# Optimization experiments

Hardware: AMD Instinct MI355X
Metric: run time of the kernel (lower is better)

Reference implementation:

```python
import jax, jax.numpy as jnp
import numpy as np


def setup_inputs() -> dict:
    key = jax.random.key(0)
    kx, kw = jax.random.split(key)
    B, C, L = 8, 512, 4096
    WC, KS = 64, 7
    x = jax.random.normal(kx, (B, C, L), dtype=jnp.float32)
    w = jax.random.normal(kw, (B, WC, KS, L), dtype=jnp.float32)
    return {"x": x, "w": w}


def reference(x, w):
    # x: [B, C, L]; w: [B, WC, KS, L]; dynamic grouped depthwise 1D conv.
    B, C, L = x.shape
    _, WC, KS, _ = w.shape
    groups = C // WC
    pad = (KS - 1) // 2
    xp = jnp.pad(x, ((0, 0), (0, 0), (pad, pad)))  # [B, C, L+2*pad]
    # repeat_interleave along channel dim: output channel c uses w channel c // groups
    wf = jnp.repeat(w, groups, axis=1) if groups > 1 else w  # [B, C, KS, L]
    # out[b,c,l] = sum_k xp[b,c,l+k] * wf[b,c,k,l]
    out = jnp.zeros((B, C, L), dtype=x.dtype)
    for k in range(KS):  # KS is a small static constant (7)
        out = out + xp[:, :, k:k + L] * wf[:, :, k, :]
    return out
```

## Files before the change

kernel.cpp:

```cpp
#include <hip/hip_runtime.h>

#define B_      8
#define C_      512
#define L_      4096
#define WC_     64
#define KS_     7
#define GROUPS_ 8
#define PAD_    3
#define LTILE_  1024
#define NTILES_ 4

__global__ __launch_bounds__(256)
void SKA_40106404610132_kernel(const float* __restrict__ x,
                               const float* __restrict__ w,
                               float* __restrict__ out) {
    const int bid  = blockIdx.x;
    const int tile = bid % NTILES_;
    const int bwc  = bid / NTILES_;
    const int wc   = bwc % WC_;
    const int b    = bwc / WC_;
    const int t    = threadIdx.x;
    const int l0   = tile * LTILE_ + t * 4;

    const float* wbase = w + ((size_t)(b * WC_ + wc) * KS_) * L_ + l0;
    float wv[KS_][4];
    #pragma unroll
    for (int k = 0; k < KS_; ++k) {
        float4 f = *reinterpret_cast<const float4*>(wbase + (size_t)k * L_);
        wv[k][0] = f.x; wv[k][1] = f.y; wv[k][2] = f.z; wv[k][3] = f.w;
    }

    const size_t grp_off = (size_t)(b * C_ + wc * GROUPS_) * L_;
    const float* xgrp = x   + grp_off;
    float*       ogrp = out + grp_off;

    const bool lo_ok = (l0 >= 4);
    const bool hi_ok = (l0 + 8 <= L_);

    #pragma unroll
    for (int g = 0; g < GROUPS_; ++g) {
        const float* xrow = xgrp + (size_t)g * L_;

        float xv[12];
        {
            float4 m = *reinterpret_cast<const float4*>(xrow + l0);
            xv[4] = m.x; xv[5] = m.y; xv[6] = m.z; xv[7] = m.w;
        }
        if (lo_ok) {
            float4 lo = *reinterpret_cast<const float4*>(xrow + l0 - 4);
            xv[0] = lo.x; xv[1] = lo.y; xv[2] = lo.z; xv[3] = lo.w;
        } else {
            xv[0] = 0.f; xv[1] = 0.f; xv[2] = 0.f; xv[3] = 0.f;
        }
        if (hi_ok) {
            float4 hi = *reinterpret_cast<const float4*>(xrow + l0 + 4);
            xv[8] = hi.x; xv[9] = hi.y; xv[10] = hi.z; xv[11] = hi.w;
        } else {
            xv[8] = 0.f; xv[9] = 0.f; xv[10] = 0.f; xv[11] = 0.f;
        }

        float acc[4];
        #pragma unroll
        for (int j = 0; j < 4; ++j) {
            float s = xv[j + 1] * wv[0][j];
            #pragma unroll
            for (int k = 1; k < KS_; ++k)
                s = fmaf(xv[j + k + 1], wv[k][j], s);
            acc[j] = s;
        }

        *reinterpret_cast<float4*>(ogrp + (size_t)g * L_ + l0) =
            make_float4(acc[0], acc[1], acc[2], acc[3]);
    }
}

extern "C" void kernel_launch(void* const* d_in, const int* in_sizes, int n_in,
                              void* d_out, int out_size, void* d_ws, size_t ws_size,
                              hipStream_t stream) {
    const float* x = (const float*)d_in[0];
    const float* w = (const float*)d_in[1];
    float* out = (float*)d_out;

    const int grid = B_ * WC_ * NTILES_;
    SKA_40106404610132_kernel<<<grid, 256, 0, stream>>>(x, w, out);
}
```

Baseline: 169.4 us.

## Split channel groups across blocks and issue all loads upfront

Each block now handles 2 of the 8 channels sharing a weight row, so the grid grows fourfold. All weight and input loads are hoisted before the compute to raise memory-level parallelism, and launch bounds request higher occupancy. The cost is that each weight tile is fetched by four blocks, relying on cache to absorb the redundant traffic.

```diff
diff --git a/kernel.cpp b/kernel.cpp
--- a/kernel.cpp
+++ b/kernel.cpp
@@ -6,72 +6,78 @@
 #define WC_     64
 #define KS_     7
 #define GROUPS_ 8
-#define PAD_    3
 #define LTILE_  1024
 #define NTILES_ 4
+#define CPT_    2
 
-__global__ __launch_bounds__(256)
+__global__ __launch_bounds__(256, 4)
 void SKA_40106404610132_kernel(const float* __restrict__ x,
                                const float* __restrict__ w,
                                float* __restrict__ out) {
     const int bid  = blockIdx.x;
-    const int tile = bid % NTILES_;
-    const int bwc  = bid / NTILES_;
-    const int wc   = bwc % WC_;
-    const int b    = bwc / WC_;
+    const int tile = bid & (NTILES_ - 1);
+    const int gp   = (bid >> 2) & 3;
+    const int bwc  = bid >> 4;
+    const int wc   = bwc & (WC_ - 1);
+    const int b    = bwc >> 6;
     const int t    = threadIdx.x;
     const int l0   = tile * LTILE_ + t * 4;
 
     const float* wbase = w + ((size_t)(b * WC_ + wc) * KS_) * L_ + l0;
-    float wv[KS_][4];
-    #pragma unroll
-    for (int k = 0; k < KS_; ++k) {
-        float4 f = *reinterpret_cast<const float4*>(wbase + (size_t)k * L_);
-        wv[k][0] = f.x; wv[k][1] = f.y; wv[k][2] = f.z; wv[k][3] = f.w;
-    }
+    const float4 wq0 = *reinterpret_cast<const float4*>(wbase + 0 * L_);
+    const float4 wq1 = *reinterpret_cast<const float4*>(wbase + 1 * L_);
+    const float4 wq2 = *reinterpret_cast<const float4*>(wbase + 2 * L_);
+    const float4 wq3 = *reinterpret_cast<const float4*>(wbase + 3 * L_);
+    const float4 wq4 = *reinterpret_cast<const float4*>(wbase + 4 * L_);
+    const float4 wq5 = *reinterpret_cast<const float4*>(wbase + 5 * L_);
+    const float4 wq6 = *reinterpret_cast<const float4*>(wbase + 6 * L_);
 
-    const size_t grp_off = (size_t)(b * C_ + wc * GROUPS_) * L_;
-    const float* xgrp = x   + grp_off;
-    float*       ogrp = out + grp_off;
+    const int c0 = wc * GROUPS_ + gp * CPT_;
+    const float* xr0 = x + (size_t)(b * C_ + c0) * L_;
+    const float* xr1 = xr0 + L_;
 
     const bool lo_ok = (l0 >= 4);
     const bool hi_ok = (l0 + 8 <= L_);
+    const float4 z4 = make_float4(0.f, 0.f, 0.f, 0.f);
 
-    #pragma unroll
-    for (int g = 0; g < GROUPS_; ++g) {
-        const float* xrow = xgrp + (size_t)g * L_;
+    const float4 a_lo = lo_ok ? *reinterpret_cast<const float4*>(xr0 + l0 - 4) : z4;
+    const float4 a_md =         *reinterpret_cast<const float4*>(xr0 + l0);
+    const float4 a_hi = hi_ok ? *reinterpret_cast<const float4*>(xr0 + l0 + 4) : z4;
+    const float4 b_lo = lo_ok ? *reinterpret_cast<const float4*>(xr1 + l0 - 4) : z4;
+    const float4 b_md =         *reinterpret_cast<const float4*>(xr1 + l0);
+    const float4 b_hi = hi_ok ? *reinterpret_cast<const float4*>(xr1 + l0 + 4) : z4;
 
-        float xv[12];
-        {
-            float4 m = *reinterpret_cast<const float4*>(xrow + l0);
-            xv[4] = m.x; xv[5] = m.y; xv[6] = m.z; xv[7] = m.w;
-        }
-        if (lo_ok) {
-            float4 lo = *reinterpret_cast<const float4*>(xrow + l0 - 4);
-            xv[0] = lo.x; xv[1] = lo.y; xv[2] = lo.z; xv[3] = lo.w;
-        } else {
-            xv[0] = 0.f; xv[1] = 0.f; xv[2] = 0.f; xv[3] = 0.f;
-        }
-        if (hi_ok) {
-            float4 hi = *reinterpret_cast<const float4*>(xrow + l0 + 4);
-            xv[8] = hi.x; xv[9] = hi.y; xv[10] = hi.z; xv[11] = hi.w;
-        } else {
-            xv[8] = 0.f; xv[9] = 0.f; xv[10] = 0.f; xv[11] = 0.f;
-        }
+    float wv[KS_][4];
+    #define WSET(k, q) wv[k][0] = q.x; wv[k][1] = q.y; wv[k][2] = q.z; wv[k][3] = q.w
+    WSET(0, wq0); WSET(1, wq1); WSET(2, wq2); WSET(3, wq3);
+    WSET(4, wq4); WSET(5, wq5); WSET(6, wq6);
+    #undef WSET
 
-        float acc[4];
-        #pragma unroll
-        for (int j = 0; j < 4; ++j) {
-            float s = xv[j + 1] * wv[0][j];
-            #pragma unroll
-            for (int k = 1; k < KS_; ++k)
-                s = fmaf(xv[j + k + 1], wv[k][j], s);
-            acc[j] = s;
-        }
+    float* or0 = out + (size_t)(b * C_ + c0) * L_;
+    float* or1 = or0 + L_;
 
-        *reinterpret_cast<float4*>(ogrp + (size_t)g * L_ + l0) =
-            make_float4(acc[0], acc[1], acc[2], acc[3]);
+    #define CONV_STORE(lo, md, hi, orow)                                     \
+    {                                                                        \
+        float xe[12];                                                        \
+        xe[0] = lo.x; xe[1] = lo.y; xe[2]  = lo.z; xe[3]  = lo.w;            \
+        xe[4] = md.x; xe[5] = md.y; xe[6]  = md.z; xe[7]  = md.w;            \
+        xe[8] = hi.x; xe[9] = hi.y; xe[10] = hi.z; xe[11] = hi.w;            \
+        float acc[4];                                                        \
+        _Pragma("unroll")                                                    \
+        for (int j = 0; j < 4; ++j) {                                        \
+            float s = xe[j + 1] * wv[0][j];                                  \
+            _Pragma("unroll")                                                \
+            for (int k = 1; k < KS_; ++k)                                    \
+                s = fmaf(xe[j + k + 1], wv[k][j], s);                        \
+            acc[j] = s;                                                      \
+        }                                                                    \
+        *reinterpret_cast<float4*>(orow + l0) =                              \
+            make_float4(acc[0], acc[1], acc[2], acc[3]);                     \
     }
+
+    CONV_STORE(a_lo, a_md, a_hi, or0);
+    CONV_STORE(b_lo, b_md, b_hi, or1);
+    #undef CONV_STORE
 }
 
 extern "C" void kernel_launch(void* const* d_in, const int* in_sizes, int n_in,
@@ -81,6 +87,6 @@
     const float* w = (const float*)d_in[1];
     float* out = (float*)d_out;
 
-    const int grid = B_ * WC_ * NTILES_;
+    const int grid = B_ * WC_ * (GROUPS_ / CPT_) * NTILES_;
     SKA_40106404610132_kernel<<<grid, 256, 0, stream>>>(x, w, out);
 }
```

New measurement: 167.9 us. About the same (-0.9%).

## Pipeline weight tiles through LDS with async global-to-LDS loads across L tiles

Applied to the files above, without the earlier changes.

Each block now handles a whole (batch, weight-channel) row across all four L tiles instead of one tile. Weights for the next tile are prefetched into a double-buffered LDS array using global_load_lds, while all 24 x loads are issued up front and consumed in order under manual vmcnt waits. The goal is to overlap memory latency across tiles and channels and raise memory-level parallelism per thread. In exchange the grid is a quarter the size (512 blocks), register pressure rises, and correctness depends on hand-counted vmcnt values, with no barrier between LDS writes by one wave and reads, which is only safe because each wave reads its own slice.

```diff
diff --git a/kernel.cpp b/kernel.cpp
--- a/kernel.cpp
+++ b/kernel.cpp
@@ -1,77 +1,123 @@
 #include <hip/hip_runtime.h>
 
-#define B_      8
-#define C_      512
-#define L_      4096
-#define WC_     64
-#define KS_     7
-#define GROUPS_ 8
-#define PAD_    3
-#define LTILE_  1024
-#define NTILES_ 4
+#define B_     8
+#define C_     512
+#define L_     4096
+#define WC_    64
+#define KS_    7
+#define G_     8
+#define TILE_  1024
+#define NT_    4
 
-__global__ __launch_bounds__(256)
+template<int N>
+__device__ __forceinline__ void waitvm() {
+    asm volatile("s_waitcnt vmcnt(%0)" :: "n"(N) : "memory");
+}
+
+__device__ __forceinline__ void gload_lds16(const float* src, float* dst) {
+    __builtin_amdgcn_global_load_lds(
+        (const __attribute__((address_space(1))) void*)src,
+        (__attribute__((address_space(3))) void*)dst, 16, 0, 0);
+}
+
+template<bool HAS_NEXT, int PRE_WAIT>
+__device__ __forceinline__ void do_tile(const float* __restrict__ xbase,
+                                        float* __restrict__ obase,
+                                        const float* __restrict__ wg,
+                                        float (*wlds)[KS_][TILE_],
+                                        int buf, int tile,
+                                        int wvc, int lane) {
+    const int l0 = tile * TILE_ + wvc + lane * 4;
+    const int lo_off = (l0 == 0)       ? l0 : l0 - 4;
+    const int hi_off = (l0 == L_ - 4)  ? l0 : l0 + 4;
+
+    float4 lo[G_], md[G_], hi[G_];
+    #pragma unroll
+    for (int g = 0; g < G_; ++g) {
+        const float* xr = xbase + (size_t)g * L_;
+        lo[g] = *reinterpret_cast<const float4*>(xr + lo_off);
+        md[g] = *reinterpret_cast<const float4*>(xr + l0);
+        hi[g] = *reinterpret_cast<const float4*>(xr + hi_off);
+    }
+    asm volatile("" ::: "memory");
+
+    if (HAS_NEXT) {
+        #pragma unroll
+        for (int k = 0; k < KS_; ++k)
+            gload_lds16(wg + (size_t)k * L_ + (tile + 1) * TILE_ + wvc + lane * 4,
+                        &wlds[buf ^ 1][k][wvc]);
+    }
+    asm volatile("" ::: "memory");
+
+    waitvm<PRE_WAIT>();
+
+    float4 wf[KS_];
+    #pragma unroll
+    for (int k = 0; k < KS_; ++k)
+        wf[k] = *reinterpret_cast<const float4*>(&wlds[buf][k][wvc + lane * 4]);
+
+    const bool lo_z = (l0 == 0);
+    const bool hi_z = (l0 == L_ - 4);
+    const float4 z4 = make_float4(0.f, 0.f, 0.f, 0.f);
+
+    #define CHAN(gi)                                                          \
+    {                                                                         \
+        waitvm<(HAS_NEXT ? 28 : 21) - 2 * gi>();                              \
+        float4 Lq = lo[gi]; if (lo_z) Lq = z4;                                \
+        float4 Mq = md[gi];                                                   \
+        float4 Hq = hi[gi]; if (hi_z) Hq = z4;                                \
+        const float xe1 = Lq.y, xe2 = Lq.z, xe3 = Lq.w;                       \
+        const float xe4 = Mq.x, xe5 = Mq.y, xe6 = Mq.z, xe7 = Mq.w;           \
+        const float xe8 = Hq.x, xe9 = Hq.y, xe10 = Hq.z;                      \
+        float ax = xe1 * wf[0].x, ay = xe2 * wf[0].y,                         \
+              az = xe3 * wf[0].z, aw = xe4 * wf[0].w;                         \
+        ax = fmaf(xe2, wf[1].x, ax); ay = fmaf(xe3, wf[1].y, ay);             \
+        az = fmaf(xe4, wf[1].z, az); aw = fmaf(xe5, wf[1].w, aw);             \
+        ax = fmaf(xe3, wf[2].x, ax); ay = fmaf(xe4, wf[2].y, ay);             \
+        az = fmaf(xe5, wf[2].z, az); aw = fmaf(xe6, wf[2].w, aw);             \
+        ax = fmaf(xe4, wf[3].x, ax); ay = fmaf(xe5, wf[3].y, ay);             \
+        az = fmaf(xe6, wf[3].z, az); aw = fmaf(xe7, wf[3].w, aw);             \
+        ax = fmaf(xe5, wf[4].x, ax); ay = fmaf(xe6, wf[4].y, ay);             \
+        az = fmaf(xe7, wf[4].z, az); aw = fmaf(xe8, wf[4].w, aw);             \
+        ax = fmaf(xe6, wf[5].x, ax); ay = fmaf(xe7, wf[5].y, ay);             \
+        az = fmaf(xe8, wf[5].z, az); aw = fmaf(xe9, wf[5].w, aw);             \
+        ax = fmaf(xe7, wf[6].x, ax); ay = fmaf(xe8, wf[6].y, ay);             \
+        az = fmaf(xe9, wf[6].z, az); aw = fmaf(xe10, wf[6].w, aw);            \
+        *reinterpret_cast<float4*>(obase + (size_t)gi * L_ + l0) =            \
+            make_float4(ax, ay, az, aw);                                      \
+        asm volatile("" ::: "memory");                                        \
+    }
+    CHAN(0) CHAN(1) CHAN(2) CHAN(3) CHAN(4) CHAN(5) CHAN(6) CHAN(7)
+    #undef CHAN
+}
+
+__global__ __launch_bounds__(256, 2)
 void SKA_40106404610132_kernel(const float* __restrict__ x,
                                const float* __restrict__ w,
                                float* __restrict__ out) {
+    __shared__ float wlds[2][KS_][TILE_];
+
     const int bid  = blockIdx.x;
-    const int tile = bid % NTILES_;
-    const int bwc  = bid / NTILES_;
-    const int wc   = bwc % WC_;
-    const int b    = bwc / WC_;
-    const int t    = threadIdx.x;
-    const int l0   = tile * LTILE_ + t * 4;
+    const int wc   = bid & (WC_ - 1);
+    const int b    = bid >> 6;
+    const int tid  = threadIdx.x;
+    const int wv   = tid >> 6;
+    const int lane = tid & 63;
+    const int wvc  = wv << 8;
 
-    const float* wbase = w + ((size_t)(b * WC_ + wc) * KS_) * L_ + l0;
-    float wv[KS_][4];
-    #pragma unroll
-    for (int k = 0; k < KS_; ++k) {
-        float4 f = *reinterpret_cast<const float4*>(wbase + (size_t)k * L_);
-        wv[k][0] = f.x; wv[k][1] = f.y; wv[k][2] = f.z; wv[k][3] = f.w;
-    }
-
-    const size_t grp_off = (size_t)(b * C_ + wc * GROUPS_) * L_;
-    const float* xgrp = x   + grp_off;
-    float*       ogrp = out + grp_off;
-
-    const bool lo_ok = (l0 >= 4);
-    const bool hi_ok = (l0 + 8 <= L_);
+    const float* xbase = x   + (size_t)(b * C_ + wc * G_) * L_;
+    float*       obase = out + (size_t)(b * C_ + wc * G_) * L_;
+    const float* wg    = w   + (size_t)(b * WC_ + wc) * KS_ * L_;
 
     #pragma unroll
-    for (int g = 0; g < GROUPS_; ++g) {
-        const float* xrow = xgrp + (size_t)g * L_;
+    for (int k = 0; k < KS_; ++k)
+        gload_lds16(wg + (size_t)k * L_ + wvc + lane * 4, &wlds[0][k][wvc]);
+    asm volatile("" ::: "memory");
 
-        float xv[12];
-        {
-            float4 m = *reinterpret_cast<const float4*>(xrow + l0);
-            xv[4] = m.x; xv[5] = m.y; xv[6] = m.z; xv[7] = m.w;
-        }
-        if (lo_ok) {
-            float4 lo = *reinterpret_cast<const float4*>(xrow + l0 - 4);
-            xv[0] = lo.x; xv[1] = lo.y; xv[2] = lo.z; xv[3] = lo.w;
-        } else {
-            xv[0] = 0.f; xv[1] = 0.f; xv[2] = 0.f; xv[3] = 0.f;
-        }
-        if (hi_ok) {
-            float4 hi = *reinterpret_cast<const float4*>(xrow + l0 + 4);
-            xv[8] = hi.x; xv[9] = hi.y; xv[10] = hi.z; xv[11] = hi.w;
-        } else {
-            xv[8] = 0.f; xv[9] = 0.f; xv[10] = 0.f; xv[11] = 0.f;
-        }
-
-        float acc[4];
-        #pragma unroll
-        for (int j = 0; j < 4; ++j) {
-            float s = xv[j + 1] * wv[0][j];
-            #pragma unroll
-            for (int k = 1; k < KS_; ++k)
-                s = fmaf(xv[j + k + 1], wv[k][j], s);
-            acc[j] = s;
-        }
-
-        *reinterpret_cast<float4*>(ogrp + (size_t)g * L_ + l0) =
-            make_float4(acc[0], acc[1], acc[2], acc[3]);
-    }
+    do_tile<true,  31>(xbase, obase, wg, wlds, 0, 0, wvc, lane);
+    do_tile<true,  39>(xbase, obase, wg, wlds, 1, 1, wvc, lane);
+    do_tile<true,  39>(xbase, obase, wg, wlds, 0, 2, wvc, lane);
+    do_tile<false, 32>(xbase, obase, wg, wlds, 1, 3, wvc, lane);
 }
 
 extern "C" void kernel_launch(void* const* d_in, const int* in_sizes, int n_in,
@@ -81,6 +127,5 @@
     const float* w = (const float*)d_in[1];
     float* out = (float*)d_out;
 
-    const int grid = B_ * WC_ * NTILES_;
-    SKA_40106404610132_kernel<<<grid, 256, 0, stream>>>(x, w, out);
+    SKA_40106404610132_kernel<<<B_ * WC_, 256, 0, stream>>>(x, w, out);
 }
```

Measured after the change: 170.4 us. No clear change (+0.6%).

## Stage x tile with halos and weights in shared memory before convolution

Applied to the files above, without the earlier changes.

Each block now loads its 8-row x tile (with 4-element halos) and the 7 weight rows into LDS, synchronizes, and then computes outputs from LDS. This replaces the three overlapping global float4 loads per row per thread, aiming to cut redundant global/L2 traffic in favour of fully coalesced single loads. It also adds launch_bounds occupancy hint of 2. The costs are about 61KB of LDS per block, which limits how many blocks fit per CU, and a barrier that keeps loads from overlapping compute.

```diff
diff --git a/kernel.cpp b/kernel.cpp
--- a/kernel.cpp
+++ b/kernel.cpp
@@ -1,76 +1,103 @@
 #include <hip/hip_runtime.h>
 
-#define B_      8
-#define C_      512
-#define L_      4096
-#define WC_     64
-#define KS_     7
-#define GROUPS_ 8
-#define PAD_    3
-#define LTILE_  1024
-#define NTILES_ 4
+#define B_     8
+#define C_     512
+#define L_     4096
+#define WC_    64
+#define KS_    7
+#define G_     8
+#define TILE_  1024
+#define NT_    4
+#define XSTR_  1032
 
-__global__ __launch_bounds__(256)
+__global__ __launch_bounds__(256, 2)
 void SKA_40106404610132_kernel(const float* __restrict__ x,
                                const float* __restrict__ w,
                                float* __restrict__ out) {
+    __shared__ float xs[G_][XSTR_];
+    __shared__ float ws_[KS_][TILE_];
+
     const int bid  = blockIdx.x;
-    const int tile = bid % NTILES_;
-    const int bwc  = bid / NTILES_;
-    const int wc   = bwc % WC_;
-    const int b    = bwc / WC_;
+    const int tile = bid & (NT_ - 1);
+    const int wc   = (bid >> 2) & (WC_ - 1);
+    const int b    = bid >> 8;
     const int t    = threadIdx.x;
-    const int l0   = tile * LTILE_ + t * 4;
 
-    const float* wbase = w + ((size_t)(b * WC_ + wc) * KS_) * L_ + l0;
-    float wv[KS_][4];
-    #pragma unroll
-    for (int k = 0; k < KS_; ++k) {
-        float4 f = *reinterpret_cast<const float4*>(wbase + (size_t)k * L_);
-        wv[k][0] = f.x; wv[k][1] = f.y; wv[k][2] = f.z; wv[k][3] = f.w;
+    const size_t grp = (size_t)(b * C_ + wc * G_) * L_;
+    const float* xg  = x + grp + tile * TILE_;
+    const float* wg  = w + ((size_t)(b * WC_ + wc) * KS_) * L_ + tile * TILE_;
+
+    {
+        const int r  = t >> 5;
+        const int c4 = (t & 31) * 4;
+        const float* xr = xg + (size_t)r * L_;
+        float* xsr = &xs[r][4];
+        #pragma unroll
+        for (int i = 0; i < 8; ++i) {
+            const int col = c4 + i * 128;
+            *reinterpret_cast<float4*>(xsr + col) =
+                *reinterpret_cast<const float4*>(xr + col);
+        }
+    }
+    if (t < 8) {
+        const float4 z4 = make_float4(0.f, 0.f, 0.f, 0.f);
+        *reinterpret_cast<float4*>(&xs[t][0]) =
+            (tile > 0) ? *reinterpret_cast<const float4*>(xg + (size_t)t * L_ - 4)
+                       : z4;
+    } else if (t < 16) {
+        const int r = t - 8;
+        const float4 z4 = make_float4(0.f, 0.f, 0.f, 0.f);
+        *reinterpret_cast<float4*>(&xs[r][4 + TILE_]) =
+            (tile < NT_ - 1)
+                ? *reinterpret_cast<const float4*>(xg + (size_t)r * L_ + TILE_)
+                : z4;
+    }
+    {
+        const int c4 = t * 4;
+        #pragma unroll
+        for (int k = 0; k < KS_; ++k)
+            *reinterpret_cast<float4*>(&ws_[k][c4]) =
+                *reinterpret_cast<const float4*>(wg + (size_t)k * L_ + c4);
     }
 
-    const size_t grp_off = (size_t)(b * C_ + wc * GROUPS_) * L_;
-    const float* xgrp = x   + grp_off;
-    float*       ogrp = out + grp_off;
+    __syncthreads();
 
-    const bool lo_ok = (l0 >= 4);
-    const bool hi_ok = (l0 + 8 <= L_);
+    const int c4 = t * 4;
+    float4 wf[KS_];
+    #pragma unroll
+    for (int k = 0; k < KS_; ++k)
+        wf[k] = *reinterpret_cast<const float4*>(&ws_[k][c4]);
+
+    float* og = out + grp + tile * TILE_;
 
     #pragma unroll
-    for (int g = 0; g < GROUPS_; ++g) {
-        const float* xrow = xgrp + (size_t)g * L_;
+    for (int g = 0; g < G_; ++g) {
+        const float* base = &xs[g][c4];
+        const float4 lo = *reinterpret_cast<const float4*>(base);
+        const float4 md = *reinterpret_cast<const float4*>(base + 4);
+        const float4 hi = *reinterpret_cast<const float4*>(base + 8);
 
-        float xv[12];
-        {
-            float4 m = *reinterpret_cast<const float4*>(xrow + l0);
-            xv[4] = m.x; xv[5] = m.y; xv[6] = m.z; xv[7] = m.w;
-        }
-        if (lo_ok) {
-            float4 lo = *reinterpret_cast<const float4*>(xrow + l0 - 4);
-            xv[0] = lo.x; xv[1] = lo.y; xv[2] = lo.z; xv[3] = lo.w;
-        } else {
-            xv[0] = 0.f; xv[1] = 0.f; xv[2] = 0.f; xv[3] = 0.f;
-        }
-        if (hi_ok) {
-            float4 hi = *reinterpret_cast<const float4*>(xrow + l0 + 4);
-            xv[8] = hi.x; xv[9] = hi.y; xv[10] = hi.z; xv[11] = hi.w;
-        } else {
-            xv[8] = 0.f; xv[9] = 0.f; xv[10] = 0.f; xv[11] = 0.f;
-        }
+        const float xe1 = lo.y, xe2 = lo.z, xe3 = lo.w;
+        const float xe4 = md.x, xe5 = md.y, xe6 = md.z, xe7 = md.w;
+        const float xe8 = hi.x, xe9 = hi.y, xe10 = hi.z;
 
-        float acc[4];
-        #pragma unroll
-        for (int j = 0; j < 4; ++j) {
-            float s = xv[j + 1] * wv[0][j];
-            #pragma unroll
-            for (int k = 1; k < KS_; ++k)
-                s = fmaf(xv[j + k + 1], wv[k][j], s);
-            acc[j] = s;
-        }
+        float ax = xe1 * wf[0].x, ay = xe2 * wf[0].y,
+              az = xe3 * wf[0].z, aw = xe4 * wf[0].w;
+        ax = fmaf(xe2, wf[1].x, ax); ay = fmaf(xe3, wf[1].y, ay);
+        az = fmaf(xe4, wf[1].z, az); aw = fmaf(xe5, wf[1].w, aw);
+        ax = fmaf(xe3, wf[2].x, ax); ay = fmaf(xe4, wf[2].y, ay);
+        az = fmaf(xe5, wf[2].z, az); aw = fmaf(xe6, wf[2].w, aw);
+        ax = fmaf(xe4, wf[3].x, ax); ay = fmaf(xe5, wf[3].y, ay);
+        az = fmaf(xe6, wf[3].z, az); aw = fmaf(xe7, wf[3].w, aw);
+        ax = fmaf(xe5, wf[4].x, ax); ay = fmaf(xe6, wf[4].y, ay);
+        az = fmaf(xe7, wf[4].z, az); aw = fmaf(xe8, wf[4].w, aw);
+        ax = fmaf(xe6, wf[5].x, ax); ay = fmaf(xe7, wf[5].y, ay);
+        az = fmaf(xe8, wf[5].z, az); aw = fmaf(xe9, wf[5].w, aw);
+        ax = fmaf(xe7, wf[6].x, ax); ay = fmaf(xe8, wf[6].y, ay);
+        az = fmaf(xe9, wf[6].z, az); aw = fmaf(xe10, wf[6].w, aw);
 
-        *reinterpret_cast<float4*>(ogrp + (size_t)g * L_ + l0) =
-            make_float4(acc[0], acc[1], acc[2], acc[3]);
+        *reinterpret_cast<float4*>(og + (size_t)g * L_ + c4) =
+            make_float4(ax, ay, az, aw);
     }
 }
 
@@ -81,6 +108,5 @@
     const float* w = (const float*)d_in[1];
     float* out = (float*)d_out;
 
-    const int grid = B_ * WC_ * NTILES_;
-    SKA_40106404610132_kernel<<<grid, 256, 0, stream>>>(x, w, out);
+    SKA_40106404610132_kernel<<<B_ * WC_ * NT_, 256, 0, stream>>>(x, w, out);
 }
```

Result: faster. 164.4 us (-2.9%).
